# Kernel tuning notes

Hardware: AMD Instinct MI355X
Metric: run time of the kernel (lower is better)

## Reference

```python
import jax, jax.numpy as jnp
import numpy as np

BLANK = 4
NEG = -1.0e30  # log-space 'zero'


def _ctc_loss(log_probs, targets, input_lengths, target_lengths):
    # log_probs: (N, T, C) raw logits -> module applies log_softmax then transposes to (T, N, C)
    lp = jax.nn.log_softmax(log_probs, axis=-1)
    lp = jnp.transpose(lp, (1, 0, 2))  # (T, N, C)
    T, N, C = lp.shape
    S = targets.shape[1]
    L = 2 * S + 1  # extended label length (blanks interleaved)

    # extended label sequence: blank, y1, blank, y2, ..., yS, blank  -> (N, L)
    ext = jnp.full((N, L), BLANK, dtype=targets.dtype).at[:, 1::2].set(targets)

    # gather per-step log-probs of extended labels: (T, N, L)
    lp_ext = jnp.take_along_axis(lp, jnp.broadcast_to(ext[None], (T, N, L)), axis=2)

    # skip transition (k-2 -> k) allowed iff ext[k] != blank and ext[k] != ext[k-2]
    ext_m2 = jnp.pad(ext[:, :-2], ((0, 0), (2, 0)), constant_values=BLANK)
    skip = (ext != BLANK) & (ext != ext_m2)
    skip = skip.at[:, :2].set(False)

    # alpha at t=0: only positions 0 (blank) and 1 (first label) reachable
    alpha0 = jnp.full((N, L), NEG, dtype=lp.dtype)
    alpha0 = alpha0.at[:, 0].set(lp_ext[0, :, 0]).at[:, 1].set(lp_ext[0, :, 1])

    neg_col = jnp.full((N, 1), NEG, dtype=lp.dtype)

    def step(alpha, xs):
        t, lpe = xs  # lpe: (N, L)
        s1 = jnp.concatenate([neg_col, alpha[:, :-1]], axis=1)
        s2 = jnp.concatenate([neg_col, neg_col, alpha[:, :-2]], axis=1)
        a = jnp.logaddexp(alpha, s1)
        a = jnp.logaddexp(a, jnp.where(skip, s2, NEG))
        new = a + lpe
        # freeze alpha once past this sequence's input length
        alpha = jnp.where((t < input_lengths)[:, None], new, alpha)
        return alpha, None

    ts = jnp.arange(1, T)
    alpha, _ = jax.lax.scan(step, alpha0, (ts, lp_ext[1:]))

    idx = jnp.arange(N)
    last = 2 * target_lengths  # final blank position; last label is at 2L-1
    l_label = alpha[idx, last - 1]
    l_blank = alpha[idx, last]
    nll = -jnp.logaddexp(l_label, l_blank)  # per-sequence negative log-likelihood

    # reduction='mean': divide each loss by its target length, then mean over batch
    return jnp.mean(nll / target_lengths.astype(nll.dtype))


def setup_inputs() -> dict:
    key = jax.random.key(0)
    k1, k2, k3, k4 = jax.random.split(key, 4)
    N, T, C, S = 32, 1600, 1024, 200
    log_probs = jax.random.normal(k1, (N, T, C), dtype=jnp.float32)
    # targets in [0, C) excluding blank index 4
    t = jax.random.randint(k2, (N, S), 0, C - 1)
    targets = t + (t >= BLANK).astype(t.dtype)
    input_lengths = jax.random.randint(k3, (N,), 800, T + 1)
    target_lengths = jax.random.randint(k4, (N,), 50, S + 1)
    return {
        "log_probs": log_probs,
        "targets": targets,
        "input_lengths": input_lengths,
        "target_lengths": target_lengths,
    }


def reference(log_probs, targets, input_lengths, target_lengths):
    return _ctc_loss(log_probs, targets, input_lengths, target_lengths)
```

## Files before the change

kernel.cpp:

```cpp
#include <hip/hip_runtime.h>
#include <hip/hip_bf16.h>

#define N_    32
#define T_    1600
#define C_    1024
#define S_    200
#define L_    401
#define LP_   512
#define BLANK_ 4
#define LN2_  0.69314718055994531f
#define L2E_  1.44269504088896341f
#define DPF   8

#if __has_builtin(__builtin_amdgcn_exp2f)
#define EXP2(x) __builtin_amdgcn_exp2f(x)
#else
#define EXP2(x) exp2f(x)
#endif
#if __has_builtin(__builtin_amdgcn_rcpf)
#define RCP(x) __builtin_amdgcn_rcpf(x)
#else
#define RCP(x) (1.0f / (x))
#endif

__global__ __launch_bounds__(256)
void k_softmax_gather(const float* __restrict__ logits,
                      const int* __restrict__ targets,
                      const int* __restrict__ tgt_len,
                      float* __restrict__ P) {
  const int row  = blockIdx.x * 4 + (threadIdx.x >> 6);
  const int lane = threadIdx.x & 63;
  const int wv   = threadIdx.x >> 6;
  const int n    = row / T_;
  const float* x = logits + (size_t)row * C_;
  __shared__ float sh[4][C_];

  float4 v[4];
#pragma unroll
  for (int i = 0; i < 4; ++i)
    v[i] = reinterpret_cast<const float4*>(x)[i * 64 + lane];

  float mx = v[0].x;
#pragma unroll
  for (int i = 0; i < 4; ++i)
    mx = fmaxf(mx, fmaxf(fmaxf(v[i].x, v[i].y), fmaxf(v[i].z, v[i].w)));
#pragma unroll
  for (int i = 1; i < 64; i <<= 1) mx = fmaxf(mx, __shfl_xor(mx, i));

  float s = 0.0f;
#pragma unroll
  for (int i = 0; i < 4; ++i) {
    s += EXP2((v[i].x - mx) * L2E_) + EXP2((v[i].y - mx) * L2E_)
       + EXP2((v[i].z - mx) * L2E_) + EXP2((v[i].w - mx) * L2E_);
  }
#pragma unroll
  for (int i = 1; i < 64; i <<= 1) s += __shfl_xor(s, i);
  float rz = RCP(s);

#pragma unroll
  for (int i = 0; i < 4; ++i)
    reinterpret_cast<float4*>(sh[wv])[i * 64 + lane] = v[i];
  __syncthreads();

  const int* tg = targets + n * S_;
  const int lmax = 2 * tgt_len[n];
  float* out = P + (size_t)row * LP_;
#pragma unroll
  for (int i = 0; i < 8; ++i) {
    int l = lane + i * 64;
    float p = 0.0f;
    if (l <= lmax) {
      int c = (l & 1) ? tg[(l - 1) >> 1] : BLANK_;
      p = EXP2((sh[wv][c] - mx) * L2E_) * rz;
    }
    out[l] = p;
  }
}

__global__ __launch_bounds__(64, 1)
void k_ctc(const float* __restrict__ P,
           const int* __restrict__ targets,
           const int* __restrict__ in_len,
           const int* __restrict__ tgt_len,
           float* __restrict__ nll_out) {
  const int n = blockIdx.x;
  const int lane = threadIdx.x;
  const int Tn = in_len[n];
  const float* g = P + (size_t)n * T_ * LP_;
  const int* tg = targets + n * S_;

  const int m0 = lane * 4;
  auto skv = [&](int m) -> float {
    int mi = (m >= 1 && m < S_) ? m : 1;
    return (m >= 1 && m < S_ && tg[mi] != tg[mi - 1]) ? 1.0f : 0.0f;
  };
  const float sk1 = skv(m0), sk3 = skv(m0 + 1);
  const float sk5 = skv(m0 + 2), sk7 = skv(m0 + 3);

  float a0 = 0.0f, a1 = 0.0f, a2 = 0.0f, a3 = 0.0f;
  float a4 = 0.0f, a5 = 0.0f, a6 = 0.0f, a7 = 0.0f;
  float up = 0.0f;
  if (lane == 0) { a0 = g[0]; a1 = g[1]; }
  int Etot = 0;

  const float* gl = g + lane * 8;
  const int src = (lane + 63) & 63;

  auto step = [&](const float4& A, const float4& B) {
    float a7n = (a7 + a6 + sk7 * a5) * B.w;
    float a6n = (a6 + a5) * B.z;
    float upn = __shfl(a7n, src);
    float a5n = (a5 + a4 + sk5 * a3) * B.y;
    float a4n = (a4 + a3) * B.x;
    float a3n = (a3 + a2 + sk3 * a1) * A.w;
    float a2n = (a2 + a1) * A.z;
    float a1n = (a1 + a0 + sk1 * up) * A.y;
    float a0n = (a0 + up) * A.x;
    if (lane == 0) upn = 0.0f;
    a0 = a0n; a1 = a1n; a2 = a2n; a3 = a3n;
    a4 = a4n; a5 = a5n; a6 = a6n; a7 = a7n;
    up = upn;
  };

  auto renorm = [&]() {
    float m = fmaxf(fmaxf(fmaxf(a0, a1), fmaxf(a2, a3)),
                    fmaxf(fmaxf(a4, a5), fmaxf(a6, a7)));
#pragma unroll
    for (int i = 1; i < 64; i <<= 1) m = fmaxf(m, __shfl_xor(m, i));
    int R = 125 - ((__float_as_int(m) >> 23) & 0xFF);
    a0 = ldexpf(a0, R); a1 = ldexpf(a1, R); a2 = ldexpf(a2, R);
    a3 = ldexpf(a3, R); a4 = ldexpf(a4, R); a5 = ldexpf(a5, R);
    a6 = ldexpf(a6, R); a7 = ldexpf(a7, R);
    up = ldexpf(up, R);
    Etot -= R;
  };

  auto ld = [&](int tt, float4& A, float4& B) {
    if (tt > T_ - 1) tt = T_ - 1;
    const float* p = gl + (size_t)tt * LP_;
    A = *reinterpret_cast<const float4*>(p);
    B = *reinterpret_cast<const float4*>(p + 4);
  };

  float4 A0[DPF], B0[DPF], A1[DPF], B1[DPF];
#pragma unroll
  for (int d = 0; d < DPF; ++d) ld(1 + d, A0[d], B0[d]);

  int t = 1;
  int rem = Tn - 1;
  while (rem >= 2 * DPF) {
#pragma unroll
    for (int d = 0; d < DPF; ++d) ld(t + DPF + d, A1[d], B1[d]);
#pragma unroll
    for (int d = 0; d < DPF; ++d) {
      step(A0[d], B0[d]);
      if ((d & 3) == 3) renorm();
    }
    t += DPF;
#pragma unroll
    for (int d = 0; d < DPF; ++d) ld(t + DPF + d, A0[d], B0[d]);
#pragma unroll
    for (int d = 0; d < DPF; ++d) {
      step(A1[d], B1[d]);
      if ((d & 3) == 3) renorm();
    }
    t += DPF;
    rem -= 2 * DPF;
  }
  if (rem >= DPF) {
#pragma unroll
    for (int d = 0; d < DPF; ++d) ld(t + DPF + d, A1[d], B1[d]);
#pragma unroll
    for (int d = 0; d < DPF; ++d) {
      step(A0[d], B0[d]);
      if ((d & 3) == 3) renorm();
    }
    t += DPF; rem -= DPF;
#pragma unroll
    for (int d = 0; d < DPF; ++d) {
      if (d < rem) step(A1[d], B1[d]);
      if ((d & 3) == 3) renorm();
    }
  } else {
#pragma unroll
    for (int d = 0; d < DPF; ++d) {
      if (d < rem) step(A0[d], B0[d]);
      if ((d & 3) == 3) renorm();
    }
  }

  __shared__ float sa[LP_];
  sa[lane * 8 + 0] = a0; sa[lane * 8 + 1] = a1;
  sa[lane * 8 + 2] = a2; sa[lane * 8 + 3] = a3;
  sa[lane * 8 + 4] = a4; sa[lane * 8 + 5] = a5;
  sa[lane * 8 + 6] = a6; sa[lane * 8 + 7] = a7;
  __syncthreads();
  if (lane == 0) {
    int tl = tgt_len[n];
    double v = (double)sa[2 * tl - 1] + (double)sa[2 * tl];
    int ee;
    double mfr = frexp(v, &ee);
    nll_out[n] = -LN2_ * ((float)(Etot + ee) + log2f((float)mfr));
  }
}

__global__ void k_final(const float* __restrict__ nll,
                        const int* __restrict__ tgt_len,
                        float* __restrict__ out) {
  int lane = threadIdx.x;
  float v = 0.0f;
  if (lane < N_) v = nll[lane] / (float)tgt_len[lane];
#pragma unroll
  for (int i = 1; i < 64; i <<= 1) v += __shfl_xor(v, i);
  if (lane == 0) out[0] = v * (1.0f / N_);
}

__global__ void k_sentinel(float* out) { out[0] = -12345.0f; }

extern "C" void kernel_launch(void* const* d_in, const int* in_sizes, int n_in,
                              void* d_out, int out_size, void* d_ws, size_t ws_size,
                              hipStream_t stream) {
  const float* logits = (const float*)d_in[0];
  const int* targets  = (const int*)d_in[1];
  const int* in_len   = (const int*)d_in[2];
  const int* tgt_len  = (const int*)d_in[3];
  float* out = (float*)d_out;

  size_t gbytes = (size_t)N_ * T_ * LP_ * sizeof(float);
  if (ws_size < gbytes + 256) {
    k_sentinel<<<1, 1, 0, stream>>>(out);
    return;
  }
  float* G = (float*)d_ws;
  float* nll = (float*)((char*)d_ws + gbytes);

  k_softmax_gather<<<(N_ * T_) / 4, 256, 0, stream>>>(logits, targets, tgt_len, G);
  k_ctc<<<N_, 64, 0, stream>>>(G, targets, in_len, tgt_len, nll);
  k_final<<<1, 64, 0, stream>>>(nll, tgt_len, out);
}
```

Measured before the change: 523.2 us.

## Replace wave-wide renorm reduction with per-lane exponents in CTC alpha recursion

Each lane now keeps its own scaling exponent for its 8 alpha values instead of sharing one exponent across the wave. This removes the 6-step cross-lane max reduction from every renorm. The lane's exponent is shuffled along with the boundary alpha, and the incoming neighbour value is rescaled to the local exponent. In exchange each step does an extra integer shuffle, an ldexp, and a conditional rebase of all eight values when exponents drift apart, and the final combine has to reconcile two exponents.

```diff
diff --git a/kernel.cpp b/kernel.cpp
--- a/kernel.cpp
+++ b/kernel.cpp
@@ -21,6 +21,11 @@
 #define RCP(x) __builtin_amdgcn_rcpf(x)
 #else
 #define RCP(x) (1.0f / (x))
+#endif
+#if __has_builtin(__builtin_amdgcn_ldexpf)
+#define LDX(x, e) __builtin_amdgcn_ldexpf((x), (e))
+#else
+#define LDX(x, e) ldexpf((x), (e))
 #endif
 
 __global__ __launch_bounds__(256)
@@ -100,39 +105,44 @@
   float a0 = 0.0f, a1 = 0.0f, a2 = 0.0f, a3 = 0.0f;
   float a4 = 0.0f, a5 = 0.0f, a6 = 0.0f, a7 = 0.0f;
   float up = 0.0f;
+  int   E = 0;
+  int   Eup = 0;
   if (lane == 0) { a0 = g[0]; a1 = g[1]; }
-  int Etot = 0;
 
   const float* gl = g + lane * 8;
   const int src = (lane + 63) & 63;
 
   auto step = [&](const float4& A, const float4& B) {
+    int D = Eup - E;
+    if (D > 64 && up != 0.0f) {
+      a0 = LDX(a0, -D); a1 = LDX(a1, -D); a2 = LDX(a2, -D); a3 = LDX(a3, -D);
+      a4 = LDX(a4, -D); a5 = LDX(a5, -D); a6 = LDX(a6, -D); a7 = LDX(a7, -D);
+      E = Eup; D = 0;
+    }
+    float u = LDX(up, D);
     float a7n = (a7 + a6 + sk7 * a5) * B.w;
     float a6n = (a6 + a5) * B.z;
     float upn = __shfl(a7n, src);
+    int  Eupn = __shfl(E, src);
     float a5n = (a5 + a4 + sk5 * a3) * B.y;
     float a4n = (a4 + a3) * B.x;
     float a3n = (a3 + a2 + sk3 * a1) * A.w;
     float a2n = (a2 + a1) * A.z;
-    float a1n = (a1 + a0 + sk1 * up) * A.y;
-    float a0n = (a0 + up) * A.x;
+    float a1n = (a1 + a0 + sk1 * u) * A.y;
+    float a0n = (a0 + u) * A.x;
     if (lane == 0) upn = 0.0f;
     a0 = a0n; a1 = a1n; a2 = a2n; a3 = a3n;
     a4 = a4n; a5 = a5n; a6 = a6n; a7 = a7n;
-    up = upn;
+    up = upn; Eup = Eupn;
   };
 
   auto renorm = [&]() {
     float m = fmaxf(fmaxf(fmaxf(a0, a1), fmaxf(a2, a3)),
                     fmaxf(fmaxf(a4, a5), fmaxf(a6, a7)));
-#pragma unroll
-    for (int i = 1; i < 64; i <<= 1) m = fmaxf(m, __shfl_xor(m, i));
     int R = 125 - ((__float_as_int(m) >> 23) & 0xFF);
-    a0 = ldexpf(a0, R); a1 = ldexpf(a1, R); a2 = ldexpf(a2, R);
-    a3 = ldexpf(a3, R); a4 = ldexpf(a4, R); a5 = ldexpf(a5, R);
-    a6 = ldexpf(a6, R); a7 = ldexpf(a7, R);
-    up = ldexpf(up, R);
-    Etot -= R;
+    a0 = LDX(a0, R); a1 = LDX(a1, R); a2 = LDX(a2, R); a3 = LDX(a3, R);
+    a4 = LDX(a4, R); a5 = LDX(a5, R); a6 = LDX(a6, R); a7 = LDX(a7, R);
+    E -= R;
   };
 
   auto ld = [&](int tt, float4& A, float4& B) {
@@ -190,17 +200,23 @@
   }
 
   __shared__ float sa[LP_];
+  __shared__ int   se[LP_];
   sa[lane * 8 + 0] = a0; sa[lane * 8 + 1] = a1;
   sa[lane * 8 + 2] = a2; sa[lane * 8 + 3] = a3;
   sa[lane * 8 + 4] = a4; sa[lane * 8 + 5] = a5;
   sa[lane * 8 + 6] = a6; sa[lane * 8 + 7] = a7;
+#pragma unroll
+  for (int j = 0; j < 8; ++j) se[lane * 8 + j] = E;
   __syncthreads();
   if (lane == 0) {
     int tl = tgt_len[n];
-    double v = (double)sa[2 * tl - 1] + (double)sa[2 * tl];
+    float v1 = sa[2 * tl - 1], v2 = sa[2 * tl];
+    int   E1 = se[2 * tl - 1], E2 = se[2 * tl];
+    int   Em = max(E1, E2);
+    double v = ldexp((double)v1, E1 - Em) + ldexp((double)v2, E2 - Em);
     int ee;
     double mfr = frexp(v, &ee);
-    nll_out[n] = -LN2_ * ((float)(Etot + ee) + log2f((float)mfr));
+    nll_out[n] = -LN2_ * ((float)(Em + ee) + log2f((float)mfr));
   }
 }
 
```

Measured after the change: 506.8 us. 3.1% less time.
